# Kernel tuning notes

Hardware: AMD Instinct MI355X
Metric: run time of the kernel (lower is better)

Reference implementation:

```python
import jax, jax.numpy as jnp
import numpy as np
import math

NUM_HEADS = 8

def _ln(x, g, b, eps=1e-5):
    mu = x.mean(-1, keepdims=True)
    var = ((x - mu) ** 2).mean(-1, keepdims=True)
    return (x - mu) / jnp.sqrt(var + eps) * g + b

def setup_inputs() -> dict:
    key = jax.random.key(0)
    ks = jax.random.split(key, 10)
    B, Nq, Nk, dQ, dK, dV = 16, 1024, 1024, 512, 512, 512
    s = 0.05  # small init so the double-exp in masked_softmax stays finite
    Q = jax.random.normal(ks[0], (B, Nq, dQ), jnp.float32)
    K = jax.random.normal(ks[1], (B, Nk, dK), jnp.float32)
    Qm = (jax.random.uniform(ks[2], (B, Nq, 1)) < 0.9).astype(jnp.float32)
    Km = (jax.random.uniform(ks[3], (B, Nk, 1)) < 0.9).astype(jnp.float32)
    Wq = jax.random.normal(ks[4], (dQ, dV), jnp.float32) * s
    Wk = jax.random.normal(ks[5], (dK, dV), jnp.float32) * s
    Wv = jax.random.normal(ks[6], (dK, dV), jnp.float32) * s
    Wo = jax.random.normal(ks[7], (dV, dV), jnp.float32) * s
    bq = jnp.zeros((dV,), jnp.float32); bk = jnp.zeros((dV,), jnp.float32)
    bv = jnp.zeros((dV,), jnp.float32); bo = jnp.zeros((dV,), jnp.float32)
    g0 = jnp.ones((dV,), jnp.float32); b0 = jnp.zeros((dV,), jnp.float32)
    g1 = jnp.ones((dV,), jnp.float32); b1 = jnp.zeros((dV,), jnp.float32)
    return {"Q": Q, "K": K, "Qm": Qm, "Km": Km,
            "Wq": Wq, "bq": bq, "Wk": Wk, "bk": bk, "Wv": Wv, "bv": bv,
            "Wo": Wo, "bo": bo, "g0": g0, "b0": b0, "g1": g1, "b1": b1}

def reference(Q, K, Qm, Km, Wq, bq, Wk, bk, Wv, bv, Wo, bo, g0, b0, g1, b1):
    B, Nq, _ = Q.shape
    Nk = K.shape[1]
    dV = Wq.shape[1]
    h = NUM_HEADS
    dh = dV // h
    # projections + feature masking (Qm/Km broadcast over feature dim)
    Qp = (Q @ Wq + bq) * Qm          # [B,Nq,dV]
    Kp = (K @ Wk + bk) * Km          # [B,Nk,dV]
    V  = K @ Wv + bv                 # [B,Nk,dV]
    # head split: torch.cat(split(dh,2),0) == head-major [h,B,N,dh]
    Qh = Qp.reshape(B, Nq, h, dh).transpose(2, 0, 1, 3)
    Kh = Kp.reshape(B, Nk, h, dh).transpose(2, 0, 1, 3)
    Vh = V.reshape(B, Nk, h, dh).transpose(2, 0, 1, 3)
    S = jnp.einsum('hbqd,hbkd->hbqk', Qh, Kh) / math.sqrt(dV)
    # faithful masked_softmax: exp applied twice (Km branch then Qm branch)
    X = jnp.exp(S) * Km[:, :, 0][None, :, None, :]   # [h,B,Nq,Nk]
    X = jnp.exp(X) * Qm[:, :, 0][None, :, :, None]
    A = X / (X.sum(-1, keepdims=True) + 1e-8)
    O = Qh + jnp.einsum('hbqk,hbkd->hbqd', A, Vh)    # residual in head space
    O = O.transpose(1, 2, 0, 3).reshape(B, Nq, dV)   # merge heads back
    O = _ln(O, g0, b0)
    O = O + jax.nn.relu(O @ Wo + bo)
    return _ln(O, g1, b1)
```

## Files before the change

kernel.cpp:

```cpp
#include <hip/hip_runtime.h>
#include <hip/hip_bf16.h>
#include <cstdint>


typedef __bf16 bf16;
typedef __bf16 bf16x4 __attribute__((ext_vector_type(4)));
typedef __bf16 bf16x8 __attribute__((ext_vector_type(8)));
typedef float f32x4 __attribute__((ext_vector_type(4)));

#define MFMA16(a, b, c) __builtin_amdgcn_mfma_f32_16x16x32_bf16((a), (b), (c), 0, 0, 0)

#if __has_builtin(__builtin_amdgcn_exp2f)
#define EXP2F(x) __builtin_amdgcn_exp2f(x)
#else
#define EXP2F(x) exp2f(x)
#endif

static __device__ __forceinline__ void async_lds16(const bf16* g, bf16* l) {
  __builtin_amdgcn_global_load_lds(
      (__attribute__((address_space(1))) void*)(void*)g,
      (__attribute__((address_space(3))) void*)l,
      16, 0, 0);
}

__global__ __launch_bounds__(256) void transposeW(
    const float* __restrict__ Wq, const float* __restrict__ Wk,
    const float* __restrict__ Wv, const float* __restrict__ Wo,
    bf16* __restrict__ Tq, bf16* __restrict__ Tk,
    bf16* __restrict__ Tv, bf16* __restrict__ To) {
  const float* src;
  bf16* dst;
  switch (blockIdx.z) {
    case 0: src = Wq; dst = Tq; break;
    case 1: src = Wk; dst = Tk; break;
    case 2: src = Wv; dst = Tv; break;
    default: src = Wo; dst = To; break;
  }
  __shared__ bf16 t[64][72];
  const int tid = threadIdx.x;
  const int n0 = blockIdx.x * 64;
  const int k0 = blockIdx.y * 64;
  for (int c = tid; c < 512; c += 256) {
    const int row = c >> 3, col = (c & 7) * 8;
    const float* sp = src + (size_t)(k0 + row) * 512 + n0 + col;
    const f32x4 a = *(const f32x4*)sp;
    const f32x4 b = *(const f32x4*)(sp + 4);
    bf16x8 v;
#pragma unroll
    for (int j = 0; j < 4; ++j) { v[j] = (bf16)a[j]; v[j + 4] = (bf16)b[j]; }
    *(bf16x8*)(&t[row][col]) = v;
  }
  __syncthreads();
  for (int c = tid; c < 512; c += 256) {
    const int row = c >> 3, col8 = (c & 7) * 8;
    bf16x8 v;
#pragma unroll
    for (int j = 0; j < 8; ++j) v[j] = t[col8 + j][row];
    *(bf16x8*)(dst + (size_t)(n0 + row) * 512 + k0 + col8) = v;
  }
}

struct ConvArgs {
  const float* src[10];
  bf16* dst[10];
  int n[10];
};

__global__ __launch_bounds__(256) void convert_all(ConvArgs a) {
  const int seg = blockIdx.z;
  const int n = a.n[seg];
  const long i = ((long)blockIdx.x * 256 + threadIdx.x) * 8;
  if (i >= n) return;
  const float* s = a.src[seg];
  const f32x4 x0 = *(const f32x4*)(s + i);
  const f32x4 x1 = *(const f32x4*)(s + i + 4);
  bf16x8 o;
#pragma unroll
  for (int j = 0; j < 4; ++j) { o[j] = (bf16)x0[j]; o[j + 4] = (bf16)x1[j]; }
  *(bf16x8*)(a.dst[seg] + i) = o;
}

__global__ __launch_bounds__(256) void transposeV(
    const bf16* __restrict__ V, bf16* __restrict__ Vt) {
  __shared__ bf16 t[64][72];
  const int tid = threadIdx.x;
  const int kk0 = blockIdx.x * 64;
  const int d0 = blockIdx.y * 64;
  const int b = blockIdx.z;
  const bf16* src = V + ((long)b * 1024 + kk0) * 512 + d0;
  for (int c = tid; c < 512; c += 256) {
    const int row = c >> 3, col = (c & 7) * 8;
    *(bf16x8*)(&t[row][col]) = *(const bf16x8*)(src + (long)row * 512 + col);
  }
  __syncthreads();
  bf16* dst = Vt + ((long)b * 8 + (d0 >> 6)) * 64 * 1024 + kk0;
  for (int c = tid; c < 512; c += 256) {
    const int drow = c >> 3, col8 = (c & 7) * 8;
    bf16x8 v;
#pragma unroll
    for (int j = 0; j < 8; ++j) v[j] = t[col8 + j][drow];
    *(bf16x8*)(dst + (long)drow * 1024 + col8) = v;
  }
}

template <bool AF32>
__global__ __launch_bounds__(256) void gemm512(
    const void* __restrict__ A, const bf16* __restrict__ Bt,
    const bf16* __restrict__ bias, const bf16* __restrict__ mask,
    const bf16* __restrict__ resid, bf16* __restrict__ out) {
  __shared__ bf16 sA[128 * 32];
  __shared__ bf16 sB[128 * 32];
  const int tid = threadIdx.x;
  const int lane = tid & 63;
  const int w = tid >> 6;
  const int fm = lane & 15;
  const int fq = lane >> 4;
  const long rowBase = (long)blockIdx.y * 128;
  const int colBase = blockIdx.x * 128;

  f32x4 acc[4][4] = {};

  const int c0 = tid, c1 = tid + 256;
  const int r0 = c0 >> 2, o0 = (c0 & 3) * 8;
  const int r1 = c1 >> 2, o1 = (c1 & 3) * 8;
  const bf16* A0 = (const bf16*)A + (rowBase + r0) * 512 + o0;
  const bf16* A1 = (const bf16*)A + (rowBase + r1) * 512 + o1;
  const float* F0 = (const float*)A + (rowBase + r0) * 512 + o0;
  const float* F1 = (const float*)A + (rowBase + r1) * 512 + o1;
  const bf16* B0 = Bt + (size_t)(colBase + r0) * 512 + o0;
  const bf16* B1 = Bt + (size_t)(colBase + r1) * 512 + o1;

  const int wr = (w & 1) * 64;
  const int wc = (w >> 1) * 64;

  f32x4 nx0, nx1, ny0, ny1;
  if (AF32) {
    nx0 = *(const f32x4*)(F0);
    nx1 = *(const f32x4*)(F0 + 4);
    ny0 = *(const f32x4*)(F1);
    ny1 = *(const f32x4*)(F1 + 4);
  }

  for (int kt = 0; kt < 16; ++kt) {
    const int k0 = kt * 32;
    __syncthreads();
    if (AF32) {
      bf16x8 p, q;
#pragma unroll
      for (int j = 0; j < 4; ++j) {
        p[j] = (bf16)nx0[j]; p[j + 4] = (bf16)nx1[j];
        q[j] = (bf16)ny0[j]; q[j + 4] = (bf16)ny1[j];
      }
      *(bf16x8*)(sA + c0 * 8) = p;
      *(bf16x8*)(sA + c1 * 8) = q;
      if (kt < 15) {
        nx0 = *(const f32x4*)(F0 + k0 + 32);
        nx1 = *(const f32x4*)(F0 + k0 + 36);
        ny0 = *(const f32x4*)(F1 + k0 + 32);
        ny1 = *(const f32x4*)(F1 + k0 + 36);
      }
    } else {
      async_lds16(A0 + k0, sA + c0 * 8);
      async_lds16(A1 + k0, sA + c1 * 8);
    }
    async_lds16(B0 + k0, sB + c0 * 8);
    async_lds16(B1 + k0, sB + c1 * 8);
    __syncthreads();
    bf16x8 a[4], b[4];
#pragma unroll
    for (int i = 0; i < 4; ++i)
      a[i] = *(const bf16x8*)(sA + (wr + i * 16 + fm) * 32 + fq * 8);
#pragma unroll
    for (int j = 0; j < 4; ++j)
      b[j] = *(const bf16x8*)(sB + (wc + j * 16 + fm) * 32 + fq * 8);
#pragma unroll
    for (int i = 0; i < 4; ++i)
#pragma unroll
      for (int j = 0; j < 4; ++j)
        acc[i][j] = MFMA16(a[i], b[j], acc[i][j]);
  }

#pragma unroll
  for (int i = 0; i < 4; ++i) {
#pragma unroll
    for (int r = 0; r < 4; ++r) {
      const long R = rowBase + wr + i * 16 + fq * 4 + r;
      const float mk = mask ? (float)mask[R] : 1.0f;
      const bf16* resrow = resid ? resid + R * 512 : nullptr;
      bf16* outrow = out + R * 512;
#pragma unroll
      for (int j = 0; j < 4; ++j) {
        const int C = colBase + wc + j * 16 + fm;
        float v = acc[i][j][r] + (float)bias[C];
        if (mask) v *= mk;
        if (resid) v = (float)resrow[C] + fmaxf(v, 0.0f);
        outrow[C] = (bf16)v;
      }
    }
  }
}

__global__ __launch_bounds__(256) void attn_kernel(
    bf16* __restrict__ Qp, const bf16* __restrict__ Kp,
    const bf16* __restrict__ Vt, const bf16* __restrict__ Qm,
    const bf16* __restrict__ Km) {
  __shared__ bf16 sQ[64][72];
  __shared__ bf16 sK[64][72];
  __shared__ bf16 sVt[64][72];
  __shared__ bf16 sX[4][16][72];
  __shared__ float sKl[64];
  __shared__ float sL[4][16];

  const int tid = threadIdx.x;
  const int lane = tid & 63;
  const int w = tid >> 6;
  const int fm = lane & 15;
  const int fq = lane >> 4;
  const int q0 = blockIdx.x * 64;
  const int b = blockIdx.y;
  const int hh = blockIdx.z;

  bf16* Qbase = Qp + ((long)b * 1024 + q0) * 512 + hh * 64;
  for (int c = tid; c < 512; c += 256) {
    const int row = c >> 3, col = (c & 7) * 8;
    *(bf16x8*)(&sQ[row][col]) = *(const bf16x8*)(Qbase + (long)row * 512 + col);
  }
  const float qm_lane = (float)Qm[(long)b * 1024 + q0 + w * 16 + fm];

  f32x4 acc_o[4] = {};
  float l_lane = 0.f;
  const float c1 = 0.063758715f;
  const float LOG2E = 1.4426950408889634f;

  const bf16* Vthead = Vt + ((long)b * 8 + hh) * 64 * 1024;
  const bf16* Kbb = Kp + (long)b * 1024 * 512 + hh * 64;
  const bf16* Kmb = Km + (long)b * 1024;

  for (int kt = 0; kt < 16; ++kt) {
    const int kk0 = kt * 64;
    __syncthreads();
    const bf16* Kbase = Kbb + (long)kk0 * 512;
    for (int c = tid; c < 512; c += 256) {
      const int row = c >> 3, col = (c & 7) * 8;
      *(bf16x8*)(&sK[row][col]) = *(const bf16x8*)(Kbase + (long)row * 512 + col);
      *(bf16x8*)(&sVt[row][col]) =
          *(const bf16x8*)(Vthead + (long)row * 1024 + kk0 + col);
    }
    if (tid < 64) sKl[tid] = (float)Kmb[kk0 + tid] * LOG2E;
    __syncthreads();

    bf16x8 qf[2];
    qf[0] = *(const bf16x8*)(&sQ[w * 16 + fm][fq * 8]);
    qf[1] = *(const bf16x8*)(&sQ[w * 16 + fm][32 + fq * 8]);
    f32x4 s_acc[4] = {};
#pragma unroll
    for (int ks = 0; ks < 2; ++ks)
#pragma unroll
      for (int t = 0; t < 4; ++t) {
        const bf16x8 kf = *(const bf16x8*)(&sK[t * 16 + fm][ks * 32 + fq * 8]);
        s_acc[t] = MFMA16(kf, qf[ks], s_acc[t]);
      }
#pragma unroll
    for (int t = 0; t < 4; ++t) {
      const f32x4 kml4 = *(const f32x4*)(&sKl[t * 16 + fq * 4]);
      bf16x4 xp;
#pragma unroll
      for (int r = 0; r < 4; ++r) {
        const float e1 = EXP2F(s_acc[t][r] * c1);
        const float y = EXP2F(e1 * kml4[r]);
        l_lane += y;
        xp[r] = (bf16)y;
      }
      *(bf16x4*)((void*)&sX[w][fm][t * 16 + fq * 4]) = xp;
    }
#pragma unroll
    for (int ks = 0; ks < 2; ++ks) {
      const bf16x8 xf = *(const bf16x8*)(&sX[w][fm][ks * 32 + fq * 8]);
#pragma unroll
      for (int t = 0; t < 4; ++t) {
        const bf16x8 vf = *(const bf16x8*)(&sVt[t * 16 + fm][ks * 32 + fq * 8]);
        acc_o[t] = MFMA16(xf, vf, acc_o[t]);
      }
    }
  }

  l_lane += __shfl_xor(l_lane, 16);
  l_lane += __shfl_xor(l_lane, 32);
  if (fq == 0) sL[w][fm] = l_lane;

#pragma unroll
  for (int t = 0; t < 4; ++t) {
#pragma unroll
    for (int r = 0; r < 4; ++r) {
      const int qr = w * 16 + fq * 4 + r;
      const int dc = t * 16 + fm;
      const float qm_r = __shfl(qm_lane, fq * 4 + r, 64);
      const float li = 1.0f / (qm_r * sL[w][fq * 4 + r] + 1e-8f);
      const float val = (float)sQ[qr][dc] + qm_r * acc_o[t][r] * li;
      Qbase[(long)qr * 512 + dc] = (bf16)val;
    }
  }
}

__global__ __launch_bounds__(256) void lnorm(
    const bf16* __restrict__ X, const bf16* __restrict__ g,
    const bf16* __restrict__ bb, bf16* __restrict__ out) {
  const int row = blockIdx.x * 4 + (threadIdx.x >> 6);
  const int lane = threadIdx.x & 63;
  const bf16x8 v = *(const bf16x8*)(X + (size_t)row * 512 + lane * 8);
  float x[8], s = 0.f, ss = 0.f;
#pragma unroll
  for (int j = 0; j < 8; ++j) {
    x[j] = (float)v[j];
    s += x[j];
    ss += x[j] * x[j];
  }
#pragma unroll
  for (int m = 1; m < 64; m <<= 1) {
    s += __shfl_xor(s, m);
    ss += __shfl_xor(ss, m);
  }
  const float mean = s * (1.0f / 512.0f);
  const float var = ss * (1.0f / 512.0f) - mean * mean;
  const float rstd = 1.0f / sqrtf(var + 1e-5f);
  const bf16x8 gv = *(const bf16x8*)(g + lane * 8);
  const bf16x8 bv = *(const bf16x8*)(bb + lane * 8);
  bf16x8 o;
#pragma unroll
  for (int j = 0; j < 8; ++j)
    o[j] = (bf16)((x[j] - mean) * rstd * (float)gv[j] + (float)bv[j]);
  *(bf16x8*)(out + (size_t)row * 512 + lane * 8) = o;
}

__global__ __launch_bounds__(256) void lnorm_out(
    const bf16* __restrict__ X, const bf16* __restrict__ g,
    const bf16* __restrict__ bb, float* __restrict__ out) {
  const int row = blockIdx.x * 4 + (threadIdx.x >> 6);
  const int lane = threadIdx.x & 63;
  const bf16x8 v = *(const bf16x8*)(X + (size_t)row * 512 + lane * 8);
  float x[8], s = 0.f, ss = 0.f;
#pragma unroll
  for (int j = 0; j < 8; ++j) {
    x[j] = (float)v[j];
    s += x[j];
    ss += x[j] * x[j];
  }
#pragma unroll
  for (int m = 1; m < 64; m <<= 1) {
    s += __shfl_xor(s, m);
    ss += __shfl_xor(ss, m);
  }
  const float mean = s * (1.0f / 512.0f);
  const float var = ss * (1.0f / 512.0f) - mean * mean;
  const float rstd = 1.0f / sqrtf(var + 1e-5f);
  const bf16x8 gv = *(const bf16x8*)(g + lane * 8);
  const bf16x8 bv = *(const bf16x8*)(bb + lane * 8);
  f32x4 a, c;
#pragma unroll
  for (int j = 0; j < 4; ++j) {
    a[j] = (x[j] - mean) * rstd * (float)gv[j] + (float)bv[j];
    c[j] = (x[j + 4] - mean) * rstd * (float)gv[j + 4] + (float)bv[j + 4];
  }
  float* fo = out + (size_t)row * 512 + lane * 8;
  *(f32x4*)fo = a;
  *(f32x4*)(fo + 4) = c;
}

extern "C" void kernel_launch(void* const* d_in, const int* in_sizes, int n_in,
                              void* d_out, int out_size, void* d_ws, size_t ws_size,
                              hipStream_t stream) {
  (void)in_sizes; (void)n_in; (void)out_size; (void)ws_size;
  const float* Q = (const float*)d_in[0];
  const float* K = (const float*)d_in[1];

  bf16* ws = (bf16*)d_ws;
  const long W2 = 512L * 512;
  const long MN = 16384L * 512;
  bf16* Tq = ws;
  bf16* Tk = Tq + W2;
  bf16* Tv = Tk + W2;
  bf16* To = Tv + W2;
  bf16* sm = To + W2;
  bf16* cQm = sm + 8 * 512;
  bf16* cKm = cQm + 16384;
  bf16* Qp = cKm + 16384;
  bf16* Kp = Qp + MN;
  bf16* Vx = (bf16*)d_out;
  bf16* Vt = (bf16*)d_out + MN;

  bf16* cbq = sm + 0 * 512;
  bf16* cbk = sm + 1 * 512;
  bf16* cbv = sm + 2 * 512;
  bf16* cbo = sm + 3 * 512;
  bf16* cg0 = sm + 4 * 512;
  bf16* cb0 = sm + 5 * 512;
  bf16* cg1 = sm + 6 * 512;
  bf16* cb1 = sm + 7 * 512;

  transposeW<<<dim3(8, 8, 4), 256, 0, stream>>>(
      (const float*)d_in[4], (const float*)d_in[6],
      (const float*)d_in[8], (const float*)d_in[10], Tq, Tk, Tv, To);

  ConvArgs ca;
  ca.src[0] = (const float*)d_in[2];  ca.dst[0] = cQm; ca.n[0] = 16384;
  ca.src[1] = (const float*)d_in[3];  ca.dst[1] = cKm; ca.n[1] = 16384;
  ca.src[2] = (const float*)d_in[5];  ca.dst[2] = cbq; ca.n[2] = 512;
  ca.src[3] = (const float*)d_in[7];  ca.dst[3] = cbk; ca.n[3] = 512;
  ca.src[4] = (const float*)d_in[9];  ca.dst[4] = cbv; ca.n[4] = 512;
  ca.src[5] = (const float*)d_in[11]; ca.dst[5] = cbo; ca.n[5] = 512;
  ca.src[6] = (const float*)d_in[12]; ca.dst[6] = cg0; ca.n[6] = 512;
  ca.src[7] = (const float*)d_in[13]; ca.dst[7] = cb0; ca.n[7] = 512;
  ca.src[8] = (const float*)d_in[14]; ca.dst[8] = cg1; ca.n[8] = 512;
  ca.src[9] = (const float*)d_in[15]; ca.dst[9] = cb1; ca.n[9] = 512;
  convert_all<<<dim3(8, 1, 10), 256, 0, stream>>>(ca);

  const dim3 gg(4, 128);
  gemm512<true><<<gg, 256, 0, stream>>>(Q, Tq, cbq, cQm, nullptr, Qp);
  gemm512<true><<<gg, 256, 0, stream>>>(K, Tk, cbk, cKm, nullptr, Kp);
  gemm512<true><<<gg, 256, 0, stream>>>(K, Tv, cbv, nullptr, nullptr, Vx);

  transposeV<<<dim3(16, 8, 16), 256, 0, stream>>>(Vx, Vt);

  attn_kernel<<<dim3(16, 16, 8), 256, 0, stream>>>(Qp, Kp, Vt, cQm, cKm);

  lnorm<<<4096, 256, 0, stream>>>(Qp, cg0, cb0, Qp);
  gemm512<false><<<gg, 256, 0, stream>>>(Qp, To, cbo, nullptr, Qp, Kp);
  lnorm_out<<<4096, 256, 0, stream>>>(Kp, cg1, cb1, (float*)d_out);
}
```

Baseline: 343.6 us.

## Fuse K and V projections into one GEMM writing transposed V directly

Replaces the separate K and V projection GEMMs and the V transpose kernel with one gemmKV kernel. It reads the fp32 K input once, computes both projections, and writes V straight into the head-major transposed layout that attention consumes, removing a read of K, a V round-trip through memory and two launches. It also flattens the attention grid so the batch-head index varies fastest, hoists the Q fragment loads out of the key loop, and adds min-blocks-per-SM launch bounds to gemm512. The fused kernel holds two accumulator sets, so register pressure rises and occupancy may drop. Its transposed V stores are 8-byte scattered writes.

```diff
diff --git a/kernel.cpp b/kernel.cpp
--- a/kernel.cpp
+++ b/kernel.cpp
@@ -80,31 +80,8 @@
   *(bf16x8*)(a.dst[seg] + i) = o;
 }
 
-__global__ __launch_bounds__(256) void transposeV(
-    const bf16* __restrict__ V, bf16* __restrict__ Vt) {
-  __shared__ bf16 t[64][72];
-  const int tid = threadIdx.x;
-  const int kk0 = blockIdx.x * 64;
-  const int d0 = blockIdx.y * 64;
-  const int b = blockIdx.z;
-  const bf16* src = V + ((long)b * 1024 + kk0) * 512 + d0;
-  for (int c = tid; c < 512; c += 256) {
-    const int row = c >> 3, col = (c & 7) * 8;
-    *(bf16x8*)(&t[row][col]) = *(const bf16x8*)(src + (long)row * 512 + col);
-  }
-  __syncthreads();
-  bf16* dst = Vt + ((long)b * 8 + (d0 >> 6)) * 64 * 1024 + kk0;
-  for (int c = tid; c < 512; c += 256) {
-    const int drow = c >> 3, col8 = (c & 7) * 8;
-    bf16x8 v;
-#pragma unroll
-    for (int j = 0; j < 8; ++j) v[j] = t[col8 + j][drow];
-    *(bf16x8*)(dst + (long)drow * 1024 + col8) = v;
-  }
-}
-
 template <bool AF32>
-__global__ __launch_bounds__(256) void gemm512(
+__global__ __launch_bounds__(256, 2) void gemm512(
     const void* __restrict__ A, const bf16* __restrict__ Bt,
     const bf16* __restrict__ bias, const bf16* __restrict__ mask,
     const bf16* __restrict__ resid, bf16* __restrict__ out) {
@@ -200,6 +177,113 @@
   }
 }
 
+__global__ __launch_bounds__(256, 2) void gemmKV(
+    const float* __restrict__ A, const bf16* __restrict__ Btk,
+    const bf16* __restrict__ Btv, const bf16* __restrict__ bk,
+    const bf16* __restrict__ bv, const bf16* __restrict__ Km,
+    bf16* __restrict__ Kp, bf16* __restrict__ Vt) {
+  __shared__ bf16 sA[128 * 32];
+  __shared__ bf16 sBk[128 * 32];
+  __shared__ bf16 sBv[128 * 32];
+  const int tid = threadIdx.x;
+  const int lane = tid & 63;
+  const int w = tid >> 6;
+  const int fm = lane & 15;
+  const int fq = lane >> 4;
+  const long rowBase = (long)blockIdx.y * 128;
+  const int colBase = blockIdx.x * 128;
+
+  f32x4 acck[4][4] = {};
+  f32x4 accv[4][4] = {};
+
+  const int c0 = tid, c1 = tid + 256;
+  const int r0 = c0 >> 2, o0 = (c0 & 3) * 8;
+  const int r1 = c1 >> 2, o1 = (c1 & 3) * 8;
+  const float* F0 = A + (rowBase + r0) * 512 + o0;
+  const float* F1 = A + (rowBase + r1) * 512 + o1;
+  const bf16* Bk0 = Btk + (size_t)(colBase + r0) * 512 + o0;
+  const bf16* Bk1 = Btk + (size_t)(colBase + r1) * 512 + o1;
+  const bf16* Bv0 = Btv + (size_t)(colBase + r0) * 512 + o0;
+  const bf16* Bv1 = Btv + (size_t)(colBase + r1) * 512 + o1;
+
+  const int wr = (w & 1) * 64;
+  const int wc = (w >> 1) * 64;
+
+  f32x4 nx0 = *(const f32x4*)(F0);
+  f32x4 nx1 = *(const f32x4*)(F0 + 4);
+  f32x4 ny0 = *(const f32x4*)(F1);
+  f32x4 ny1 = *(const f32x4*)(F1 + 4);
+
+  for (int kt = 0; kt < 16; ++kt) {
+    const int k0 = kt * 32;
+    __syncthreads();
+    {
+      bf16x8 p, q;
+#pragma unroll
+      for (int j = 0; j < 4; ++j) {
+        p[j] = (bf16)nx0[j]; p[j + 4] = (bf16)nx1[j];
+        q[j] = (bf16)ny0[j]; q[j + 4] = (bf16)ny1[j];
+      }
+      *(bf16x8*)(sA + c0 * 8) = p;
+      *(bf16x8*)(sA + c1 * 8) = q;
+      if (kt < 15) {
+        nx0 = *(const f32x4*)(F0 + k0 + 32);
+        nx1 = *(const f32x4*)(F0 + k0 + 36);
+        ny0 = *(const f32x4*)(F1 + k0 + 32);
+        ny1 = *(const f32x4*)(F1 + k0 + 36);
+      }
+    }
+    async_lds16(Bk0 + k0, sBk + c0 * 8);
+    async_lds16(Bk1 + k0, sBk + c1 * 8);
+    async_lds16(Bv0 + k0, sBv + c0 * 8);
+    async_lds16(Bv1 + k0, sBv + c1 * 8);
+    __syncthreads();
+    bf16x8 a[4], b[4], bv2[4];
+#pragma unroll
+    for (int i = 0; i < 4; ++i)
+      a[i] = *(const bf16x8*)(sA + (wr + i * 16 + fm) * 32 + fq * 8);
+#pragma unroll
+    for (int j = 0; j < 4; ++j) {
+      b[j] = *(const bf16x8*)(sBk + (wc + j * 16 + fm) * 32 + fq * 8);
+      bv2[j] = *(const bf16x8*)(sBv + (wc + j * 16 + fm) * 32 + fq * 8);
+    }
+#pragma unroll
+    for (int i = 0; i < 4; ++i)
+#pragma unroll
+      for (int j = 0; j < 4; ++j) {
+        acck[i][j] = MFMA16(a[i], b[j], acck[i][j]);
+        accv[i][j] = MFMA16(a[i], bv2[j], accv[i][j]);
+      }
+  }
+
+  const int bidx = (int)(rowBase >> 10);
+#pragma unroll
+  for (int i = 0; i < 4; ++i) {
+#pragma unroll
+    for (int r = 0; r < 4; ++r) {
+      const long R = rowBase + wr + i * 16 + fq * 4 + r;
+      const float mk = (float)Km[R];
+      bf16* outrow = Kp + R * 512;
+#pragma unroll
+      for (int j = 0; j < 4; ++j) {
+        const int C = colBase + wc + j * 16 + fm;
+        outrow[C] = (bf16)((acck[i][j][r] + (float)bk[C]) * mk);
+      }
+    }
+    const int kkb = (int)(rowBase & 1023) + wr + i * 16 + fq * 4;
+#pragma unroll
+    for (int j = 0; j < 4; ++j) {
+      const int C = colBase + wc + j * 16 + fm;
+      const float bvc = (float)bv[C];
+      bf16x4 pv;
+#pragma unroll
+      for (int r = 0; r < 4; ++r) pv[r] = (bf16)(accv[i][j][r] + bvc);
+      bf16* dst = Vt + ((size_t)(bidx * 8 + (C >> 6)) * 64 + (C & 63)) * 1024 + kkb;
+      *(bf16x4*)((void*)dst) = pv;
+    }
+  }
+}
+
 __global__ __launch_bounds__(256) void attn_kernel(
     bf16* __restrict__ Qp, const bf16* __restrict__ Kp,
     const bf16* __restrict__ Vt, const bf16* __restrict__ Qm,
@@ -216,9 +300,11 @@
   const int w = tid >> 6;
   const int fm = lane & 15;
   const int fq = lane >> 4;
-  const int q0 = blockIdx.x * 64;
-  const int b = blockIdx.y;
-  const int hh = blockIdx.z;
+  const int id = blockIdx.x;
+  const int bh = id & 127;
+  const int q0 = (id >> 7) * 64;
+  const int b = bh >> 3;
+  const int hh = bh & 7;
 
   bf16* Qbase = Qp + ((long)b * 1024 + q0) * 512 + hh * 64;
   for (int c = tid; c < 512; c += 256) {
@@ -226,6 +312,11 @@
     *(bf16x8*)(&sQ[row][col]) = *(const bf16x8*)(Qbase + (long)row * 512 + col);
   }
   const float qm_lane = (float)Qm[(long)b * 1024 + q0 + w * 16 + fm];
+  __syncthreads();
+
+  bf16x8 qf[2];
+  qf[0] = *(const bf16x8*)(&sQ[w * 16 + fm][fq * 8]);
+  qf[1] = *(const bf16x8*)(&sQ[w * 16 + fm][32 + fq * 8]);
 
   f32x4 acc_o[4] = {};
   float l_lane = 0.f;
@@ -249,9 +340,6 @@
     if (tid < 64) sKl[tid] = (float)Kmb[kk0 + tid] * LOG2E;
     __syncthreads();
 
-    bf16x8 qf[2];
-    qf[0] = *(const bf16x8*)(&sQ[w * 16 + fm][fq * 8]);
-    qf[1] = *(const bf16x8*)(&sQ[w * 16 + fm][32 + fq * 8]);
     f32x4 s_acc[4] = {};
 #pragma unroll
     for (int ks = 0; ks < 2; ++ks)
@@ -385,8 +473,7 @@
   bf16* cKm = cQm + 16384;
   bf16* Qp = cKm + 16384;
   bf16* Kp = Qp + MN;
-  bf16* Vx = (bf16*)d_out;
-  bf16* Vt = (bf16*)d_out + MN;
+  bf16* Vt = (bf16*)d_out;
 
   bf16* cbq = sm + 0 * 512;
   bf16* cbk = sm + 1 * 512;
@@ -416,12 +503,9 @@
 
   const dim3 gg(4, 128);
   gemm512<true><<<gg, 256, 0, stream>>>(Q, Tq, cbq, cQm, nullptr, Qp);
-  gemm512<true><<<gg, 256, 0, stream>>>(K, Tk, cbk, cKm, nullptr, Kp);
-  gemm512<true><<<gg, 256, 0, stream>>>(K, Tv, cbv, nullptr, nullptr, Vx);
-
-  transposeV<<<dim3(16, 8, 16), 256, 0, stream>>>(Vx, Vt);
-
-  attn_kernel<<<dim3(16, 16, 8), 256, 0, stream>>>(Qp, Kp, Vt, cQm, cKm);
+  gemmKV<<<gg, 256, 0, stream>>>(K, Tk, Tv, cbk, cbv, cKm, Kp, Vt);
+
+  attn_kernel<<<2048, 256, 0, stream>>>(Qp, Kp, Vt, cQm, cKm);
 
   lnorm<<<4096, 256, 0, stream>>>(Qp, cg0, cb0, Qp);
   gemm512<false><<<gg, 256, 0, stream>>>(Qp, To, cbo, nullptr, Qp, Kp);
```

After: 311.4 us. -9.4%, faster.
